# Performance work log

Hardware: AMD Instinct MI355X
Metric: run time of the kernel (lower is better)

## Reference

```python
import jax, jax.numpy as jnp
import numpy as np

EXPERT_NUM = 64
EXPERT_USE = 8
AUX_LOSS_LAMBDA = 0.01


def setup_inputs() -> dict:
    key = jax.random.key(0)
    k1, k2 = jax.random.split(key)
    h = jax.random.normal(k1, (4, 4096, 2048), dtype=jnp.float32)
    # nn.Linear(embed_dim, expert_num) weight: [expert_num, embed_dim], ~U(-1/sqrt(d), 1/sqrt(d))
    bound = 1.0 / np.sqrt(2048.0)
    W = jax.random.uniform(k2, (EXPERT_NUM, 2048), dtype=jnp.float32,
                           minval=-bound, maxval=bound)
    return {"h": h, "W": W}


def reference(h, W):
    b, s, d = h.shape
    hf = h.reshape(-1, d)                              # [b*s, d]
    logits = jnp.einsum('nd,ed->ne', hf, W)            # [b*s, E]
    scores = jax.nn.softmax(logits, axis=-1)           # [b*s, E]
    expert_scores, expert_ids = jax.lax.top_k(scores, EXPERT_USE)  # [b*s, k]
    expert_weight = expert_scores / jnp.sum(expert_scores, axis=-1, keepdims=True)
    # L2 load-balance aux loss (training mode, lambda > 0)
    seq_probs = scores.reshape(b, s, EXPERT_NUM).mean(axis=1)      # [b, E]
    aux_loss = jnp.mean(jnp.sum(seq_probs ** 2, axis=-1)) * EXPERT_NUM * AUX_LOSS_LAMBDA
    return expert_ids, expert_weight, aux_loss
```

## Files before the change

kernel.cpp:

```cpp
#include <hip/hip_runtime.h>
#include <math.h>

#define NTOK 16384
#define DIM 2048
#define NEXP 64
#define TOPK 8
#define BT 64
#define KC 64
#define NCHUNK (DIM / KC)
#define PADK 68
#define NBLK (NTOK / BT)
#define EPW 4

typedef float f2 __attribute__((ext_vector_type(2)));
typedef float f4 __attribute__((ext_vector_type(4)));

__device__ __forceinline__ f2 pk_mul_sv(f2 bs, f2 av) {
    f2 d; asm("v_pk_mul_f32 %0, %1, %2" : "=v"(d) : "s"(bs), "v"(av)); return d;
}
__device__ __forceinline__ f2 pk_add(f2 a, f2 b) {
    f2 d; asm("v_pk_add_f32 %0, %1, %2" : "=v"(d) : "v"(a), "v"(b)); return d;
}

__global__ __launch_bounds__(1024, 1) void moe_gate_np(
    const float* __restrict__ h, const float* __restrict__ W,
    float* __restrict__ out, float* __restrict__ wsum)
{
#pragma clang fp contract(off)
    __shared__ float sA[BT * PADK];
    __shared__ float lg[BT][NEXP + 2];

    const int tid  = threadIdx.x;
    const int lane = tid & 63;
    const int wv   = tid >> 6;
    const int blk  = blockIdx.x;
    const long tok0 = (long)blk * BT;
    const float* hA = h + tok0 * DIM;

    const int e0 = __builtin_amdgcn_readfirstlane(wv) * EPW;
    const float* wb = W + (long)e0 * DIM;

    const int rs = tid >> 4;
    const int cs = (tid & 15) * 4;
    f4 pa = *(const f4*)(hA + (long)rs * DIM + cs);

    f2 acc01[EPW], acc23[EPW];
    #pragma unroll
    for (int j = 0; j < EPW; ++j) { acc01[j] = (f2)(0.f); acc23[j] = (f2)(0.f); }

    for (int kc = 0; kc < NCHUNK; ++kc) {
        __syncthreads();
        *(f4*)&sA[rs * PADK + cs] = pa;
        __syncthreads();

        if (kc + 1 < NCHUNK) {
            const long ko = (long)(kc + 1) * KC;
            pa = *(const f4*)(hA + (long)rs * DIM + ko + cs);
        }

        #pragma unroll
        for (int s = 0; s < 4; ++s) {
            const int kb = kc * KC + s * 16;

            f4 B[EPW][4];
            #pragma unroll
            for (int j = 0; j < EPW; ++j)
                #pragma unroll
                for (int q = 0; q < 4; ++q)
                    B[j][q] = *(const f4*)(wb + (long)j * DIM + kb + 4 * q);

            f4 af[4];
            const float* ab = &sA[lane * PADK + s * 16];
            #pragma unroll
            for (int v = 0; v < 4; ++v) af[v] = *(const f4*)(ab + 4 * v);

            f2 alo[4], ahi[4];
            #pragma unroll
            for (int v = 0; v < 4; ++v) {
                alo[v] = __builtin_shufflevector(af[v], af[v], 0, 1);
                ahi[v] = __builtin_shufflevector(af[v], af[v], 2, 3);
            }

            #pragma unroll
            for (int j = 0; j < EPW; ++j) {
                f2 blo[4], bhi[4];
                #pragma unroll
                for (int v = 0; v < 4; ++v) {
                    blo[v] = __builtin_shufflevector(B[j][v], B[j][v], 0, 1);
                    bhi[v] = __builtin_shufflevector(B[j][v], B[j][v], 2, 3);
                }
                f2 t;
                t = pk_add(pk_mul_sv(blo[3], alo[3]), acc01[j]);
                t = pk_add(pk_mul_sv(blo[2], alo[2]), t);
                t = pk_add(pk_mul_sv(blo[1], alo[1]), t);
                acc01[j] = pk_add(pk_mul_sv(blo[0], alo[0]), t);
                t = pk_add(pk_mul_sv(bhi[3], ahi[3]), acc23[j]);
                t = pk_add(pk_mul_sv(bhi[2], ahi[2]), t);
                t = pk_add(pk_mul_sv(bhi[1], ahi[1]), t);
                acc23[j] = pk_add(pk_mul_sv(bhi[0], ahi[0]), t);
            }
        }
    }

    #pragma unroll
    for (int j = 0; j < EPW; ++j) {
        f2 s2 = pk_add(acc01[j], acc23[j]);
        lg[lane][e0 + j] = s2.x + s2.y;
    }
    __syncthreads();

    float auxacc = 0.f;

    for (int tt = 0; tt < 4; ++tt) {
        const int t = wv * 4 + tt;
        const float s = lg[t][lane];

        float m = s;
        #pragma unroll
        for (int off = 32; off >= 1; off >>= 1)
            m = fmaxf(m, __shfl_xor(m, off));

        const float p = expf(s - m);
        lg[t][lane] = p;
        __asm__ volatile("" ::: "memory");

        float r0s = lg[t][0], r1s = lg[t][1], r2s = lg[t][2], r3s = lg[t][3];
        float r4s = lg[t][4], r5s = lg[t][5], r6s = lg[t][6], r7s = lg[t][7];
        #pragma unroll
        for (int i = 1; i < 8; ++i) {
            r0s += lg[t][8 * i + 0]; r1s += lg[t][8 * i + 1];
            r2s += lg[t][8 * i + 2]; r3s += lg[t][8 * i + 3];
            r4s += lg[t][8 * i + 4]; r5s += lg[t][8 * i + 5];
            r6s += lg[t][8 * i + 6]; r7s += lg[t][8 * i + 7];
        }
        const float S = ((r0s + r1s) + (r2s + r3s)) + ((r4s + r5s) + (r6s + r7s));

        const float score = p / S;
        auxacc += score;

        float cv = score;
        float myv = 0.f;
        int   myi = 0;
        #pragma unroll
        for (int i = 0; i < TOPK; ++i) {
            float v = cv;
            int idx = lane;
            #pragma unroll
            for (int off = 32; off >= 1; off >>= 1) {
                float v2 = __shfl_xor(v, off);
                int   i2 = __shfl_xor(idx, off);
                if (v2 > v || (v2 == v && i2 < idx)) { v = v2; idx = i2; }
            }
            if (lane == i)   { myv = v; myi = idx; }
            if (lane == idx) cv = -1.f;
        }

        float S8 = 0.f;
        #pragma unroll
        for (int r = 0; r < TOPK; ++r) S8 += __shfl(myv, r);

        if (lane < TOPK) {
            const long o = (tok0 + t) * TOPK + lane;
            out[o]                     = (float)myi;
            out[(long)NTOK * TOPK + o] = myv / S8;
        }
    }

    const int b = blk >> 6;
    atomicAdd(&wsum[b * NEXP + lane], auxacc);
}

__global__ void aux_finish(const float* __restrict__ wsum, float* __restrict__ out)
{
    const int lane = threadIdx.x;
    float a = 0.f;
    #pragma unroll
    for (int b = 0; b < 4; ++b) {
        const float v = wsum[b * NEXP + lane] * (1.0f / 4096.0f);
        a = fmaf(v, v, a);
    }
    #pragma unroll
    for (int off = 32; off >= 1; off >>= 1)
        a += __shfl_xor(a, off);
    if (lane == 0)
        out[2L * NTOK * TOPK] = a * 0.25f * (float)NEXP * 0.01f;
}

extern "C" void kernel_launch(void* const* d_in, const int* in_sizes, int n_in,
                              void* d_out, int out_size, void* d_ws, size_t ws_size,
                              hipStream_t stream) {
    const float* h = (const float*)d_in[0];
    const float* W = (const float*)d_in[1];
    float* out  = (float*)d_out;
    float* wsum = (float*)d_ws;

    hipMemsetAsync(d_ws, 0, 1024, stream);
    moe_gate_np<<<NBLK, 1024, 0, stream>>>(h, W, out, wsum);
    aux_finish<<<1, 64, 0, stream>>>(wsum, out);
}
```

Baseline: 144.1 us.

## Split gate GEMM across expert halves with double-buffered LDS, separate softmax/top-k kernel

Result: slower. 164.0 us (+13.9%).

```diff
diff --git a/kernel.cpp b/kernel.cpp
--- a/kernel.cpp
+++ b/kernel.cpp
@@ -9,7 +9,6 @@
 #define KC 64
 #define NCHUNK (DIM / KC)
 #define PADK 68
-#define NBLK (NTOK / BT)
 #define EPW 4
 
 typedef float f2 __attribute__((ext_vector_type(2)));
@@ -22,40 +21,50 @@
     f2 d; asm("v_pk_add_f32 %0, %1, %2" : "=v"(d) : "v"(a), "v"(b)); return d;
 }
 
-__global__ __launch_bounds__(1024, 1) void moe_gate_np(
+__global__ __launch_bounds__(512, 4) void moe_gemm(
     const float* __restrict__ h, const float* __restrict__ W,
-    float* __restrict__ out, float* __restrict__ wsum)
+    float* __restrict__ lgout)
 {
 #pragma clang fp contract(off)
-    __shared__ float sA[BT * PADK];
-    __shared__ float lg[BT][NEXP + 2];
+    __shared__ float sA[2][BT * PADK];
 
     const int tid  = threadIdx.x;
     const int lane = tid & 63;
     const int wv   = tid >> 6;
-    const int blk  = blockIdx.x;
-    const long tok0 = (long)blk * BT;
+    const int tile = blockIdx.x >> 1;
+    const int hf   = blockIdx.x & 1;
+    const long tok0 = (long)tile * BT;
     const float* hA = h + tok0 * DIM;
 
-    const int e0 = __builtin_amdgcn_readfirstlane(wv) * EPW;
+    const int e0 = __builtin_amdgcn_readfirstlane(hf * 32 + wv * EPW);
     const float* wb = W + (long)e0 * DIM;
 
-    const int rs = tid >> 4;
-    const int cs = (tid & 15) * 4;
-    f4 pa = *(const f4*)(hA + (long)rs * DIM + cs);
-
-    f2 acc01[EPW], acc23[EPW];
-    #pragma unroll
-    for (int j = 0; j < EPW; ++j) { acc01[j] = (f2)(0.f); acc23[j] = (f2)(0.f); }
+    const int rs0 = tid >> 4;
+    const int cs0 = (tid & 15) * 4;
+
+    f4 ra = *(const f4*)(hA + (long)rs0 * DIM + cs0);
+    f4 rb = *(const f4*)(hA + (long)(rs0 + 32) * DIM + cs0);
+    *(f4*)&sA[0][rs0 * PADK + cs0]        = ra;
+    *(f4*)&sA[0][(rs0 + 32) * PADK + cs0] = rb;
+    ra = *(const f4*)(hA + (long)rs0 * DIM + KC + cs0);
+    rb = *(const f4*)(hA + (long)(rs0 + 32) * DIM + KC + cs0);
+
+    f2 a01[EPW], a23[EPW];
+    #pragma unroll
+    for (int j = 0; j < EPW; ++j) { a01[j] = (f2)(0.f); a23[j] = (f2)(0.f); }
 
     for (int kc = 0; kc < NCHUNK; ++kc) {
         __syncthreads();
-        *(f4*)&sA[rs * PADK + cs] = pa;
-        __syncthreads();
+        const int cur = kc & 1;
 
         if (kc + 1 < NCHUNK) {
-            const long ko = (long)(kc + 1) * KC;
-            pa = *(const f4*)(hA + (long)rs * DIM + ko + cs);
+            *(f4*)&sA[cur ^ 1][rs0 * PADK + cs0]        = ra;
+            *(f4*)&sA[cur ^ 1][(rs0 + 32) * PADK + cs0] = rb;
+        }
+        if (kc + 2 < NCHUNK) {
+            const long ko = (long)(kc + 2) * KC;
+            ra = *(const f4*)(hA + (long)rs0 * DIM + ko + cs0);
+            rb = *(const f4*)(hA + (long)(rs0 + 32) * DIM + ko + cs0);
         }
 
         #pragma unroll
@@ -70,7 +79,7 @@
                     B[j][q] = *(const f4*)(wb + (long)j * DIM + kb + 4 * q);
 
             f4 af[4];
-            const float* ab = &sA[lane * PADK + s * 16];
+            const float* ab = &sA[cur][lane * PADK + s * 16];
             #pragma unroll
             for (int v = 0; v < 4; ++v) af[v] = *(const f4*)(ab + 4 * v);
 
@@ -90,40 +99,186 @@
                     bhi[v] = __builtin_shufflevector(B[j][v], B[j][v], 2, 3);
                 }
                 f2 t;
-                t = pk_add(pk_mul_sv(blo[3], alo[3]), acc01[j]);
+                t = pk_add(pk_mul_sv(blo[3], alo[3]), a01[j]);
                 t = pk_add(pk_mul_sv(blo[2], alo[2]), t);
                 t = pk_add(pk_mul_sv(blo[1], alo[1]), t);
-                acc01[j] = pk_add(pk_mul_sv(blo[0], alo[0]), t);
-                t = pk_add(pk_mul_sv(bhi[3], ahi[3]), acc23[j]);
+                a01[j] = pk_add(pk_mul_sv(blo[0], alo[0]), t);
+                t = pk_add(pk_mul_sv(bhi[3], ahi[3]), a23[j]);
                 t = pk_add(pk_mul_sv(bhi[2], ahi[2]), t);
                 t = pk_add(pk_mul_sv(bhi[1], ahi[1]), t);
-                acc23[j] = pk_add(pk_mul_sv(bhi[0], ahi[0]), t);
+                a23[j] = pk_add(pk_mul_sv(bhi[0], ahi[0]), t);
             }
         }
     }
 
     #pragma unroll
     for (int j = 0; j < EPW; ++j) {
-        f2 s2 = pk_add(acc01[j], acc23[j]);
+        f2 s2 = pk_add(a01[j], a23[j]);
+        lgout[(tok0 + lane) * NEXP + e0 + j] = s2.x + s2.y;
+    }
+}
+
+__global__ __launch_bounds__(512) void softmax_topk(
+    const float* __restrict__ lgout, float* __restrict__ out,
+    float* __restrict__ wsum)
+{
+    __shared__ float ls[8][NEXP + 2];
+    const int tid  = threadIdx.x;
+    const int lane = tid & 63;
+    const int wv8  = tid >> 6;
+    const int blk  = blockIdx.x;
+    const long tok0 = (long)blk * 64;
+    float auxacc = 0.f;
+
+    for (int tt = 0; tt < 8; ++tt) {
+        const long gt = tok0 + wv8 * 8 + tt;
+        const float s = lgout[gt * NEXP + lane];
+
+        float m = s;
+        #pragma unroll
+        for (int off = 32; off >= 1; off >>= 1)
+            m = fmaxf(m, __shfl_xor(m, off));
+
+        const float p = expf(s - m);
+        ls[wv8][lane] = p;
+        __asm__ volatile("" ::: "memory");
+
+        float r0s = ls[wv8][0], r1s = ls[wv8][1], r2s = ls[wv8][2], r3s = ls[wv8][3];
+        float r4s = ls[wv8][4], r5s = ls[wv8][5], r6s = ls[wv8][6], r7s = ls[wv8][7];
+        #pragma unroll
+        for (int i = 1; i < 8; ++i) {
+            r0s += ls[wv8][8 * i + 0]; r1s += ls[wv8][8 * i + 1];
+            r2s += ls[wv8][8 * i + 2]; r3s += ls[wv8][8 * i + 3];
+            r4s += ls[wv8][8 * i + 4]; r5s += ls[wv8][8 * i + 5];
+            r6s += ls[wv8][8 * i + 6]; r7s += ls[wv8][8 * i + 7];
+        }
+        const float S = ((r0s + r1s) + (r2s + r3s)) + ((r4s + r5s) + (r6s + r7s));
+
+        const float score = p / S;
+        auxacc += score;
+
+        float cv = score;
+        float myv = 0.f;
+        int   myi = 0;
+        #pragma unroll
+        for (int i = 0; i < TOPK; ++i) {
+            float v = cv;
+            int idx = lane;
+            #pragma unroll
+            for (int off = 32; off >= 1; off >>= 1) {
+                float v2 = __shfl_xor(v, off);
+                int   i2 = __shfl_xor(idx, off);
+                if (v2 > v || (v2 == v && i2 < idx)) { v = v2; idx = i2; }
+            }
+            if (lane == i)   { myv = v; myi = idx; }
+            if (lane == idx) cv = -1.f;
+        }
+
+        float S8 = 0.f;
+        #pragma unroll
+        for (int r = 0; r < TOPK; ++r) S8 += __shfl(myv, r);
+
+        if (lane < TOPK) {
+            const long o = gt * TOPK + lane;
+            out[o]                     = (float)myi;
+            out[(long)NTOK * TOPK + o] = myv / S8;
+        }
+    }
+
+    atomicAdd(&wsum[(blk >> 6) * NEXP + lane], auxacc);
+}
+
+__global__ __launch_bounds__(1024, 1) void moe_gate_np(
+    const float* __restrict__ h, const float* __restrict__ W,
+    float* __restrict__ out, float* __restrict__ wsum)
+{
+#pragma clang fp contract(off)
+    __shared__ float sA[BT * PADK];
+    __shared__ float lg[BT][NEXP + 2];
+
+    const int tid  = threadIdx.x;
+    const int lane = tid & 63;
+    const int wv   = tid >> 6;
+    const int blk  = blockIdx.x;
+    const long tok0 = (long)blk * BT;
+    const float* hA = h + tok0 * DIM;
+
+    const int e0 = __builtin_amdgcn_readfirstlane(wv) * EPW;
+    const float* wb = W + (long)e0 * DIM;
+
+    const int rs = tid >> 4;
+    const int cs = (tid & 15) * 4;
+    f4 pa = *(const f4*)(hA + (long)rs * DIM + cs);
+
+    f2 a01[EPW], a23[EPW];
+    #pragma unroll
+    for (int j = 0; j < EPW; ++j) { a01[j] = (f2)(0.f); a23[j] = (f2)(0.f); }
+
+    for (int kc = 0; kc < NCHUNK; ++kc) {
+        __syncthreads();
+        *(f4*)&sA[rs * PADK + cs] = pa;
+        __syncthreads();
+        if (kc + 1 < NCHUNK)
+            pa = *(const f4*)(hA + (long)rs * DIM + (long)(kc + 1) * KC + cs);
+
+        #pragma unroll
+        for (int s = 0; s < 4; ++s) {
+            const int kb = kc * KC + s * 16;
+            f4 B[EPW][4];
+            #pragma unroll
+            for (int j = 0; j < EPW; ++j)
+                #pragma unroll
+                for (int q = 0; q < 4; ++q)
+                    B[j][q] = *(const f4*)(wb + (long)j * DIM + kb + 4 * q);
+            f4 af[4];
+            const float* ab = &sA[lane * PADK + s * 16];
+            #pragma unroll
+            for (int v = 0; v < 4; ++v) af[v] = *(const f4*)(ab + 4 * v);
+            f2 alo[4], ahi[4];
+            #pragma unroll
+            for (int v = 0; v < 4; ++v) {
+                alo[v] = __builtin_shufflevector(af[v], af[v], 0, 1);
+                ahi[v] = __builtin_shufflevector(af[v], af[v], 2, 3);
+            }
+            #pragma unroll
+            for (int j = 0; j < EPW; ++j) {
+                f2 blo[4], bhi[4];
+                #pragma unroll
+                for (int v = 0; v < 4; ++v) {
+                    blo[v] = __builtin_shufflevector(B[j][v], B[j][v], 0, 1);
+                    bhi[v] = __builtin_shufflevector(B[j][v], B[j][v], 2, 3);
+                }
+                f2 t;
+                t = pk_add(pk_mul_sv(blo[3], alo[3]), a01[j]);
+                t = pk_add(pk_mul_sv(blo[2], alo[2]), t);
+                t = pk_add(pk_mul_sv(blo[1], alo[1]), t);
+                a01[j] = pk_add(pk_mul_sv(blo[0], alo[0]), t);
+                t = pk_add(pk_mul_sv(bhi[3], ahi[3]), a23[j]);
+                t = pk_add(pk_mul_sv(bhi[2], ahi[2]), t);
+                t = pk_add(pk_mul_sv(bhi[1], ahi[1]), t);
+                a23[j] = pk_add(pk_mul_sv(bhi[0], ahi[0]), t);
+            }
+        }
+    }
+
+    #pragma unroll
+    for (int j = 0; j < EPW; ++j) {
+        f2 s2 = pk_add(a01[j], a23[j]);
         lg[lane][e0 + j] = s2.x + s2.y;
     }
     __syncthreads();
 
     float auxacc = 0.f;
-
     for (int tt = 0; tt < 4; ++tt) {
         const int t = wv * 4 + tt;
         const float s = lg[t][lane];
-
         float m = s;
         #pragma unroll
         for (int off = 32; off >= 1; off >>= 1)
             m = fmaxf(m, __shfl_xor(m, off));
-
         const float p = expf(s - m);
         lg[t][lane] = p;
         __asm__ volatile("" ::: "memory");
-
         float r0s = lg[t][0], r1s = lg[t][1], r2s = lg[t][2], r3s = lg[t][3];
         float r4s = lg[t][4], r5s = lg[t][5], r6s = lg[t][6], r7s = lg[t][7];
         #pragma unroll
@@ -134,10 +289,8 @@
             r6s += lg[t][8 * i + 6]; r7s += lg[t][8 * i + 7];
         }
         const float S = ((r0s + r1s) + (r2s + r3s)) + ((r4s + r5s) + (r6s + r7s));
-
         const float score = p / S;
         auxacc += score;
-
         float cv = score;
         float myv = 0.f;
         int   myi = 0;
@@ -154,20 +307,16 @@
             if (lane == i)   { myv = v; myi = idx; }
             if (lane == idx) cv = -1.f;
         }
-
         float S8 = 0.f;
         #pragma unroll
         for (int r = 0; r < TOPK; ++r) S8 += __shfl(myv, r);
-
         if (lane < TOPK) {
             const long o = (tok0 + t) * TOPK + lane;
             out[o]                     = (float)myi;
             out[(long)NTOK * TOPK + o] = myv / S8;
         }
     }
-
-    const int b = blk >> 6;
-    atomicAdd(&wsum[b * NEXP + lane], auxacc);
+    atomicAdd(&wsum[(blk >> 6) * NEXP + lane], auxacc);
 }
 
 __global__ void aux_finish(const float* __restrict__ wsum, float* __restrict__ out)
@@ -194,7 +343,15 @@
     float* out  = (float*)d_out;
     float* wsum = (float*)d_ws;
 
+    const size_t need = 4096 + (size_t)NTOK * NEXP * sizeof(float);
+
     hipMemsetAsync(d_ws, 0, 1024, stream);
-    moe_gate_np<<<NBLK, 1024, 0, stream>>>(h, W, out, wsum);
+    if (ws_size >= need) {
+        float* lgout = (float*)((char*)d_ws + 4096);
+        moe_gemm<<<(NTOK / BT) * 2, 512, 0, stream>>>(h, W, lgout);
+        softmax_topk<<<NTOK / 64, 512, 0, stream>>>(lgout, out, wsum);
+    } else {
+        moe_gate_np<<<NTOK / BT, 1024, 0, stream>>>(h, W, out, wsum);
+    }
     aux_finish<<<1, 64, 0, stream>>>(wsum, out);
 }
```
